# Kernel tuning notes

Hardware: AMD Instinct MI355X
Metric: run time of the kernel (lower is better)

## Reference

```python
import jax, jax.numpy as jnp
import numpy as np

N = 131072
F_IN = 256
FEATURES = 64
N_SOURCES = 32


def setup_inputs() -> dict:
    key = jax.random.key(0)
    k1, k2, k3 = jax.random.split(key, 3)
    x = jax.random.normal(k1, (N, F_IN), dtype=jnp.float32)
    source = jax.random.randint(k2, (N,), 0, N_SOURCES, dtype=jnp.int32)
    W = jax.random.normal(k3, (F_IN, N_SOURCES * FEATURES), dtype=jnp.float32) * (1.0 / np.sqrt(F_IN))
    b = jnp.zeros((N_SOURCES * FEATURES,), dtype=jnp.float32)
    return {"x": x, "source": source, "W": W, "b": b}


def reference(x, source, W, b):
    # Dense projection to all sources: (N, n_sources*features)
    y = jnp.dot(x, W) + b
    # Per-row gather of the slice belonging to this row's source id.
    # Equivalent to y[i, source[i]*FEATURES : (source[i]+1)*FEATURES].
    y = y.reshape(x.shape[0], N_SOURCES, FEATURES)
    out = jnp.take_along_axis(y, source[:, None, None].astype(jnp.int32), axis=1)
    return out[:, 0, :]  # (N, FEATURES)
```

## Files before the change

### kernel.cpp

```cpp
#include <hip/hip_runtime.h>

#define N_ROWS   131072
#define F_IN     256
#define FEAT     64
#define NSRC     32
#define WSTRIDE  (NSRC * FEAT)
#define NCH      32
#define CHUNK    4096
#define NCB      (N_ROWS / 256)
#define CBPC     16
#define CAPC     44
#define SEG      (CAPC + 1)
#define LCAP     320
#define TR       16
#define TPAD     66
#define WTOFF    (NCB * NSRC * SEG)
#define WTINTS   (NSRC * FEAT * F_IN / 2)

#define MCHUNK   4096
#define LCAP1    512
#define KPAD     264

typedef __attribute__((ext_vector_type(8))) short  bf16x8;
typedef __attribute__((ext_vector_type(4))) float  f32x4;

#define WAITV(N)  asm volatile("s_waitcnt vmcnt(" #N ")" ::: "memory")
#define WAITLGKM() asm volatile("s_waitcnt lgkmcnt(0)" ::: "memory")
#define SBAR()    do { __builtin_amdgcn_s_barrier(); __builtin_amdgcn_sched_barrier(0); } while (0)

__device__ __forceinline__ unsigned short f2bf(float f) {
    union { float f; unsigned u; } c; c.f = f;
    unsigned r = c.u + 0x7fffu + ((c.u >> 16) & 1u);
    return (unsigned short)(r >> 16);
}

__device__ __forceinline__ bf16x8 pack8(f32x4 f0, f32x4 f1) {
    bf16x8 a;
    a[0] = (short)f2bf(f0[0]); a[1] = (short)f2bf(f0[1]);
    a[2] = (short)f2bf(f0[2]); a[3] = (short)f2bf(f0[3]);
    a[4] = (short)f2bf(f1[0]); a[5] = (short)f2bf(f1[1]);
    a[6] = (short)f2bf(f1[2]); a[7] = (short)f2bf(f1[3]);
    return a;
}

__global__ __launch_bounds__(256)
void pack_w(const float* __restrict__ W, int* __restrict__ ws) {
    const int idx  = blockIdx.x * 256 + threadIdx.x;
    const int lane = idx & 63, kk = (idx >> 6) & 7, w = (idx >> 9) & 3, s = idx >> 11;
    const int col  = lane & 15, quad = lane >> 4;
    const int n    = s * FEAT + w * 16 + col;
    const int k0   = kk * 32 + quad * 8;
    bf16x8 v;
    #pragma unroll
    for (int j = 0; j < 8; ++j)
        v[j] = (short)f2bf(W[(size_t)(k0 + j) * WSTRIDE + n]);
    ((bf16x8*)(ws + WTOFF))[idx] = v;
}

__global__ __launch_bounds__(256)
void compact_kernel(const int* __restrict__ src, int* __restrict__ ws) {
    __shared__ int lcnt[NSRC];
    const int tid = threadIdx.x;
    if (tid < NSRC) lcnt[tid] = 0;
    __syncthreads();
    const int row = blockIdx.x * 256 + tid;
    const int s   = src[row];
    const int p   = atomicAdd(&lcnt[s], 1);
    if (p < CAPC)
        ws[blockIdx.x * (NSRC * SEG) + s * SEG + 1 + p] = row;
    __syncthreads();
    if (tid < NSRC)
        ws[blockIdx.x * (NSRC * SEG) + tid * SEG] = min(lcnt[tid], CAPC);
}

__device__ __forceinline__ void stage_tile(const float* __restrict__ x,
                                           const int* lst, int count, int tile,
                                           int w, int lane, float* Abuf) {
    #pragma unroll
    for (int i = 0; i < 4; ++i) {
        const int r  = w * 4 + i;
        const int gi = min(tile * TR + r, count - 1);
        const float* srcp = x + (size_t)lst[gi] * F_IN + ((lane ^ (r & 7)) << 2);
        __builtin_amdgcn_global_load_lds(
            (const __attribute__((address_space(1))) void*)srcp,
            (__attribute__((address_space(3))) void*)(Abuf + r * F_IN),
            16, 0, 0);
    }
}

__global__ __launch_bounds__(256, 4)
void gemm_kernel(const float* __restrict__ x, const float* __restrict__ b,
                 const int* __restrict__ ws, float* __restrict__ out) {
    __shared__ __align__(16) float A[2][TR][F_IN];
    __shared__ __align__(16) float T[TR * TPAD];
    __shared__ int lst[LCAP];
    __shared__ int scnt[CBPC];
    __shared__ int soff[CBPC + 1];

    const int tid = threadIdx.x;
    const int s   = blockIdx.x;
    const int c   = blockIdx.y;

    if (tid < CBPC)
        scnt[tid] = ws[(size_t)(c * CBPC + tid) * (NSRC * SEG) + s * SEG];
    __syncthreads();
    if (tid == 0) {
        int a = 0;
        #pragma unroll
        for (int jj = 0; jj < CBPC; ++jj) { soff[jj] = a; a += scnt[jj]; }
        soff[CBPC] = a;
    }
    __syncthreads();
    const int count = min(soff[CBPC], LCAP);
    if (count == 0) return;
    {
        const int jj = tid >> 4, i0 = tid & 15;
        const size_t base = (size_t)(c * CBPC + jj) * (NSRC * SEG) + s * SEG;
        const int cj = scnt[jj];
        for (int i = i0; i < cj; i += 16) {
            const int pos = soff[jj] + i;
            if (pos < LCAP) lst[pos] = ws[base + 1 + i];
        }
    }
    __syncthreads();

    const int lane = tid & 63, w = tid >> 6;
    const int col  = lane & 15, quad = lane >> 4;

    const int ntiles = (count + TR - 1) / TR;

    stage_tile(x, lst, count, 0, w, lane, &A[0][0][0]);

    bf16x8 bb[8];
    {
        const bf16x8* wp = (const bf16x8*)(ws + WTOFF) + ((s * 4 + w) * 8) * 64 + lane;
        #pragma unroll
        for (int kk = 0; kk < 8; ++kk) bb[kk] = wp[kk * 64];
    }
    const float bias = b[s * FEAT + w * 16 + col];

    for (int t = 0; t < ntiles; ++t) {
        if (t) WAITV(4); else WAITV(0);
        SBAR();
        if (t + 1 < ntiles)
            stage_tile(x, lst, count, t + 1, w, lane, &A[(t + 1) & 1][0][0]);

        f32x4 acc = (f32x4){0.f, 0.f, 0.f, 0.f};
        {
            const int key = col & 7;
            const float* arow = &A[t & 1][0][0] + col * F_IN;
            #pragma unroll
            for (int kk = 0; kk < 8; ++kk) {
                const int s0 = kk * 8 + quad * 2;
                const f32x4 lo = *(const f32x4*)(arow + (((s0    ) ^ key) << 2));
                const f32x4 hi = *(const f32x4*)(arow + (((s0 + 1) ^ key) << 2));
                unsigned u0, u1, u2, u3;
                asm("v_cvt_pk_bf16_f32 %0, %1, %2" : "=v"(u0) : "v"(lo[0]), "v"(lo[1]));
                asm("v_cvt_pk_bf16_f32 %0, %1, %2" : "=v"(u1) : "v"(lo[2]), "v"(lo[3]));
                asm("v_cvt_pk_bf16_f32 %0, %1, %2" : "=v"(u2) : "v"(hi[0]), "v"(hi[1]));
                asm("v_cvt_pk_bf16_f32 %0, %1, %2" : "=v"(u3) : "v"(hi[2]), "v"(hi[3]));
                union { unsigned u[4]; bf16x8 v; } cv;
                cv.u[0] = u0; cv.u[1] = u1; cv.u[2] = u2; cv.u[3] = u3;
                acc = __builtin_amdgcn_mfma_f32_16x16x32_bf16(cv.v, bb[kk], acc, 0, 0, 0);
            }
        }

        #pragma unroll
        for (int reg = 0; reg < 4; ++reg)
            T[(quad * 4 + reg) * TPAD + w * 16 + col] = acc[reg] + bias;
        WAITLGKM();
        SBAR();
        #pragma unroll
        for (int r = 0; r < 4; ++r) {
            const int gi = t * TR + w * 4 + r;
            if (gi < count)
                out[(size_t)lst[gi] * FEAT + lane] = T[(w * 4 + r) * TPAD + lane];
        }
    }
}

__global__ __launch_bounds__(256, 4)
void mono_kernel(const float* __restrict__ x, const int* __restrict__ src,
                 const float* __restrict__ W, const float* __restrict__ b,
                 float* __restrict__ out) {
    __shared__ __align__(16) unsigned short Wt[FEAT * KPAD];
    __shared__ int lst[LCAP1];
    __shared__ int cnt;
    const int tid = threadIdx.x, s = blockIdx.y, chunk0 = blockIdx.x * MCHUNK;
    if (tid == 0) cnt = 0;
    __syncthreads();
    {
        const int n = tid & 63, kp = (tid >> 6) * 2;
        #pragma unroll
        for (int k0 = 0; k0 < F_IN; k0 += 8) {
            const int k = k0 + kp;
            const float w0 = W[(size_t)k * WSTRIDE + s * FEAT + n];
            const float w1 = W[(size_t)(k + 1) * WSTRIDE + s * FEAT + n];
            *(unsigned*)&Wt[n * KPAD + k] = (unsigned)f2bf(w0) | ((unsigned)f2bf(w1) << 16);
        }
    }
    #pragma unroll
    for (int r = 0; r < MCHUNK / 256; ++r) {
        const int row = chunk0 + r * 256 + tid;
        if (src[row] == s) {
            const int p = atomicAdd(&cnt, 1);
            if (p < LCAP1) lst[p] = row;
        }
    }
    __syncthreads();
    const int count = cnt;
    if (count == 0) return;
    const int lane = tid & 63, w = tid >> 6, col = lane & 15, quad = lane >> 4;
    float bias[4];
    #pragma unroll
    for (int nt = 0; nt < 4; ++nt) bias[nt] = b[s * FEAT + nt * 16 + col];
    const int npass = (count + 63) >> 6;
    for (int pp = 0; pp < npass; ++pp) {
        const int base = pp * 64 + w * 16;
        const int ia = lst[min(base + col, count - 1)];
        const float* ap = x + (size_t)ia * F_IN + quad * 8;
        f32x4 av[16];
        #pragma unroll
        for (int kk = 0; kk < 8; ++kk) {
            av[2 * kk]     = *(const f32x4*)(ap + kk * 32);
            av[2 * kk + 1] = *(const f32x4*)(ap + kk * 32 + 4);
        }
        f32x4 acc[4];
        #pragma unroll
        for (int nt = 0; nt < 4; ++nt) acc[nt] = (f32x4){0.f, 0.f, 0.f, 0.f};
        #pragma unroll
        for (int kk = 0; kk < 8; ++kk) {
            const bf16x8 a = pack8(av[2 * kk], av[2 * kk + 1]);
            #pragma unroll
            for (int nt = 0; nt < 4; ++nt) {
                const bf16x8 bbv = *(const bf16x8*)&Wt[(nt * 16 + col) * KPAD + kk * 32 + quad * 8];
                acc[nt] = __builtin_amdgcn_mfma_f32_16x16x32_bf16(a, bbv, acc[nt], 0, 0, 0);
            }
        }
        #pragma unroll
        for (int reg = 0; reg < 4; ++reg) {
            const int gm = base + quad * 4 + reg;
            if (gm < count) {
                const int row = lst[gm];
                float* op = out + (size_t)row * FEAT;
                #pragma unroll
                for (int nt = 0; nt < 4; ++nt)
                    op[nt * 16 + col] = acc[nt][reg] + bias[nt];
            }
        }
    }
}

extern "C" void kernel_launch(void* const* d_in, const int* in_sizes, int n_in,
                              void* d_out, int out_size, void* d_ws, size_t ws_size,
                              hipStream_t stream) {
    const float* x   = (const float*)d_in[0];
    const int*   src = (const int*)d_in[1];
    const float* W   = (const float*)d_in[2];
    const float* b   = (const float*)d_in[3];
    float*       out = (float*)d_out;

    const size_t ws_needed = (size_t)(WTOFF + WTINTS) * sizeof(int);
    if (ws_size >= ws_needed) {
        int* ws = (int*)d_ws;
        pack_w<<<dim3(256), dim3(256), 0, stream>>>(W, ws);
        compact_kernel<<<dim3(NCB), dim3(256), 0, stream>>>(src, ws);
        gemm_kernel<<<dim3(NSRC, NCH), dim3(256), 0, stream>>>(x, b, ws, out);
    } else {
        mono_kernel<<<dim3(N_ROWS / MCHUNK, NSRC), dim3(256), 0, stream>>>(x, src, W, b, out);
    }
}
```

Before: 217.1 us.

## Pre-sort x rows into per-bucket bf16 buffers before the grouped GEMM

Replaces the compact kernel with count, scan and reorder passes. The reorder pass streams x row by row, converts it to bf16 and scatters each row into a contiguous per-(chunk, source) bucket in the workspace. The GEMM then stages contiguous bf16 tiles and feeds MFMA directly, with no gather and no per-tile conversion. This trades scattered fp32 row gathers for one extra write and read of x at half size plus two more launches. It also needs a much larger workspace, and if that is not available the code falls back to the mono kernel.

```diff
diff --git a/kernel.cpp b/kernel.cpp
--- a/kernel.cpp
+++ b/kernel.cpp
@@ -9,13 +9,22 @@
 #define CHUNK    4096
 #define NCB      (N_ROWS / 256)
 #define CBPC     16
-#define CAPC     44
-#define SEG      (CAPC + 1)
 #define LCAP     320
 #define TR       16
 #define TPAD     66
-#define WTOFF    (NCB * NSRC * SEG)
-#define WTINTS   (NSRC * FEAT * F_IN / 2)
+
+#define OFF_CNT   0
+#define SZ_CNT    (NCB * NSRC)
+#define OFF_SOFF  (OFF_CNT + SZ_CNT)
+#define SZ_SOFF   (NCH * NSRC * CBPC)
+#define OFF_BTOT  (OFF_SOFF + SZ_SOFF)
+#define SZ_BTOT   (NCH * NSRC)
+#define OFF_LSTG  (OFF_BTOT + SZ_BTOT)
+#define SZ_LSTG   (NCH * NSRC * LCAP)
+#define OFF_WT    (OFF_LSTG + SZ_LSTG)
+#define SZ_WT     (NSRC * FEAT * F_IN / 2)
+#define OFF_XS    (OFF_WT + SZ_WT)
+#define SZ_XS     (NCH * NSRC * LCAP * (F_IN/2))
 
 #define MCHUNK   4096
 #define LCAP1    512
@@ -24,9 +33,9 @@
 typedef __attribute__((ext_vector_type(8))) short  bf16x8;
 typedef __attribute__((ext_vector_type(4))) float  f32x4;
 
-#define WAITV(N)  asm volatile("s_waitcnt vmcnt(" #N ")" ::: "memory")
+#define WAITV(N)   asm volatile("s_waitcnt vmcnt(" #N ")" ::: "memory")
 #define WAITLGKM() asm volatile("s_waitcnt lgkmcnt(0)" ::: "memory")
-#define SBAR()    do { __builtin_amdgcn_s_barrier(); __builtin_amdgcn_sched_barrier(0); } while (0)
+#define SBAR()     do { __builtin_amdgcn_s_barrier(); __builtin_amdgcn_sched_barrier(0); } while (0)
 
 __device__ __forceinline__ unsigned short f2bf(float f) {
     union { float f; unsigned u; } c; c.f = f;
@@ -54,86 +63,133 @@
     #pragma unroll
     for (int j = 0; j < 8; ++j)
         v[j] = (short)f2bf(W[(size_t)(k0 + j) * WSTRIDE + n]);
-    ((bf16x8*)(ws + WTOFF))[idx] = v;
+    ((bf16x8*)(ws + OFF_WT))[idx] = v;
 }
 
 __global__ __launch_bounds__(256)
-void compact_kernel(const int* __restrict__ src, int* __restrict__ ws) {
+void count_kernel(const int* __restrict__ src, int* __restrict__ ws) {
     __shared__ int lcnt[NSRC];
     const int tid = threadIdx.x;
     if (tid < NSRC) lcnt[tid] = 0;
     __syncthreads();
-    const int row = blockIdx.x * 256 + tid;
-    const int s   = src[row];
-    const int p   = atomicAdd(&lcnt[s], 1);
-    if (p < CAPC)
-        ws[blockIdx.x * (NSRC * SEG) + s * SEG + 1 + p] = row;
-    __syncthreads();
-    if (tid < NSRC)
-        ws[blockIdx.x * (NSRC * SEG) + tid * SEG] = min(lcnt[tid], CAPC);
-}
-
-__device__ __forceinline__ void stage_tile(const float* __restrict__ x,
-                                           const int* lst, int count, int tile,
-                                           int w, int lane, float* Abuf) {
-    #pragma unroll
-    for (int i = 0; i < 4; ++i) {
-        const int r  = w * 4 + i;
-        const int gi = min(tile * TR + r, count - 1);
-        const float* srcp = x + (size_t)lst[gi] * F_IN + ((lane ^ (r & 7)) << 2);
-        __builtin_amdgcn_global_load_lds(
-            (const __attribute__((address_space(1))) void*)srcp,
-            (__attribute__((address_space(3))) void*)(Abuf + r * F_IN),
-            16, 0, 0);
+    atomicAdd(&lcnt[src[blockIdx.x * 256 + tid]], 1);
+    __syncthreads();
+    if (tid < NSRC) ws[OFF_CNT + blockIdx.x * NSRC + tid] = lcnt[tid];
+}
+
+__global__ __launch_bounds__(256)
+void scan_kernel(int* __restrict__ ws) {
+    const int bucket = blockIdx.x * 256 + threadIdx.x;
+    const int c = bucket >> 5, s = bucket & 31;
+    int acc = 0;
+    #pragma unroll
+    for (int j = 0; j < CBPC; ++j) {
+        ws[OFF_SOFF + bucket * CBPC + j] = acc;
+        acc += ws[OFF_CNT + (c * CBPC + j) * NSRC + s];
+    }
+    ws[OFF_BTOT + bucket] = min(acc, LCAP);
+}
+
+__global__ __launch_bounds__(256)
+void reorder_kernel(const float* __restrict__ x, const int* __restrict__ src,
+                    int* __restrict__ ws) {
+    __shared__ int slotbuf[256];
+    __shared__ int lcnt[NSRC];
+    __shared__ int sbase[NSRC];
+    __shared__ int send[NSRC];
+    const int tid = threadIdx.x;
+    const int c   = blockIdx.x >> 4;
+    const int jj  = blockIdx.x & 15;
+
+    if (tid < NSRC) {
+        lcnt[tid] = 0;
+        const int bucket = c * NSRC + tid;
+        sbase[tid] = bucket * LCAP + ws[OFF_SOFF + bucket * CBPC + jj];
+        send[tid]  = bucket * LCAP + LCAP;
+    }
+    __syncthreads();
+    {
+        const int row = blockIdx.x * 256 + tid;
+        const int s   = src[row];
+        const int p   = atomicAdd(&lcnt[s], 1);
+        int slot = sbase[s] + p;
+        if (slot >= send[s]) slot = -1;
+        slotbuf[tid] = slot;
+        if (slot >= 0) ws[OFF_LSTG + slot] = row;
+    }
+    __syncthreads();
+
+    const int w = tid >> 6, lane = tid & 63;
+    char* xs = (char*)(ws + OFF_XS);
+    #pragma unroll
+    for (int r0 = 0; r0 < 64; r0 += 8) {
+        f32x4 v[8];
+        int   sl[8];
+        #pragma unroll
+        for (int i = 0; i < 8; ++i) {
+            const int lr = w * 64 + r0 + i;
+            v[i]  = *(const f32x4*)(x + (size_t)(blockIdx.x * 256 + lr) * F_IN + lane * 4);
+            sl[i] = slotbuf[lr];
+        }
+        #pragma unroll
+        for (int i = 0; i < 8; ++i) {
+            if (sl[i] >= 0) {
+                unsigned u0, u1;
+                asm("v_cvt_pk_bf16_f32 %0, %1, %2" : "=v"(u0) : "v"(v[i][0]), "v"(v[i][1]));
+                asm("v_cvt_pk_bf16_f32 %0, %1, %2" : "=v"(u1) : "v"(v[i][2]), "v"(v[i][3]));
+                uint2 d; d.x = u0; d.y = u1;
+                *(uint2*)(xs + (size_t)sl[i] * 512 + lane * 8) = d;
+            }
+        }
     }
 }
 
 __global__ __launch_bounds__(256, 4)
-void gemm_kernel(const float* __restrict__ x, const float* __restrict__ b,
-                 const int* __restrict__ ws, float* __restrict__ out) {
-    __shared__ __align__(16) float A[2][TR][F_IN];
+void gemm_kernel(const float* __restrict__ b, const int* __restrict__ ws,
+                 float* __restrict__ out) {
+    __shared__ __align__(16) unsigned short A[2][TR][F_IN];
     __shared__ __align__(16) float T[TR * TPAD];
     __shared__ int lst[LCAP];
-    __shared__ int scnt[CBPC];
-    __shared__ int soff[CBPC + 1];
-
-    const int tid = threadIdx.x;
-    const int s   = blockIdx.x;
-    const int c   = blockIdx.y;
-
-    if (tid < CBPC)
-        scnt[tid] = ws[(size_t)(c * CBPC + tid) * (NSRC * SEG) + s * SEG];
-    __syncthreads();
-    if (tid == 0) {
-        int a = 0;
-        #pragma unroll
-        for (int jj = 0; jj < CBPC; ++jj) { soff[jj] = a; a += scnt[jj]; }
-        soff[CBPC] = a;
-    }
-    __syncthreads();
-    const int count = min(soff[CBPC], LCAP);
+
+    const int tid    = threadIdx.x;
+    const int s      = blockIdx.x;
+    const int c      = blockIdx.y;
+    const int bucket = c * NSRC + s;
+    const int count  = ws[OFF_BTOT + bucket];
     if (count == 0) return;
-    {
-        const int jj = tid >> 4, i0 = tid & 15;
-        const size_t base = (size_t)(c * CBPC + jj) * (NSRC * SEG) + s * SEG;
-        const int cj = scnt[jj];
-        for (int i = i0; i < cj; i += 16) {
-            const int pos = soff[jj] + i;
-            if (pos < LCAP) lst[pos] = ws[base + 1 + i];
-        }
-    }
-    __syncthreads();
+
+    for (int i = tid; i < count; i += 256)
+        lst[i] = ws[OFF_LSTG + bucket * LCAP + i];
 
     const int lane = tid & 63, w = tid >> 6;
     const int col  = lane & 15, quad = lane >> 4;
 
+    __syncthreads();
+
     const int ntiles = (count + TR - 1) / TR;
-
-    stage_tile(x, lst, count, 0, w, lane, &A[0][0][0]);
+    const char* xs = (const char*)(ws + OFF_XS) + (size_t)bucket * LCAP * 512;
+
+    #define STAGE(tile, buf)                                                     \
+    do {                                                                         \
+        _Pragma("unroll")                                                        \
+        for (int i = 0; i < 2; ++i) {                                            \
+            const int rl  = w * 4 + 2 * i + (lane >> 5);     \
+            const int gi  = min((tile) * TR + rl, count - 1);                    \
+            const int key = rl & 7;                                              \
+            const char* sp = xs + (size_t)gi * 512 + (((lane & 31) ^ key) << 4); \
+            __builtin_amdgcn_global_load_lds(                                    \
+                (const __attribute__((address_space(1))) void*)sp,               \
+                (__attribute__((address_space(3))) void*)                        \
+                    ((char*)&A[buf][0][0] + (w * 4 + 2 * i) * 512),              \
+                16, 0, 0);                                                       \
+        }                                                                        \
+    } while (0)
+
+    STAGE(0, 0);
 
     bf16x8 bb[8];
     {
-        const bf16x8* wp = (const bf16x8*)(ws + WTOFF) + ((s * 4 + w) * 8) * 64 + lane;
+        const bf16x8* wp = (const bf16x8*)(ws + OFF_WT) + ((s * 4 + w) * 8) * 64 + lane;
         #pragma unroll
         for (int kk = 0; kk < 8; ++kk) bb[kk] = wp[kk * 64];
     }
@@ -142,26 +198,16 @@
     for (int t = 0; t < ntiles; ++t) {
         if (t) WAITV(4); else WAITV(0);
         SBAR();
-        if (t + 1 < ntiles)
-            stage_tile(x, lst, count, t + 1, w, lane, &A[(t + 1) & 1][0][0]);
+        if (t + 1 < ntiles) STAGE(t + 1, (t + 1) & 1);
 
         f32x4 acc = (f32x4){0.f, 0.f, 0.f, 0.f};
         {
+            const char* arow = (const char*)&A[t & 1][0][0] + col * 512;
             const int key = col & 7;
-            const float* arow = &A[t & 1][0][0] + col * F_IN;
             #pragma unroll
             for (int kk = 0; kk < 8; ++kk) {
-                const int s0 = kk * 8 + quad * 2;
-                const f32x4 lo = *(const f32x4*)(arow + (((s0    ) ^ key) << 2));
-                const f32x4 hi = *(const f32x4*)(arow + (((s0 + 1) ^ key) << 2));
-                unsigned u0, u1, u2, u3;
-                asm("v_cvt_pk_bf16_f32 %0, %1, %2" : "=v"(u0) : "v"(lo[0]), "v"(lo[1]));
-                asm("v_cvt_pk_bf16_f32 %0, %1, %2" : "=v"(u1) : "v"(lo[2]), "v"(lo[3]));
-                asm("v_cvt_pk_bf16_f32 %0, %1, %2" : "=v"(u2) : "v"(hi[0]), "v"(hi[1]));
-                asm("v_cvt_pk_bf16_f32 %0, %1, %2" : "=v"(u3) : "v"(hi[2]), "v"(hi[3]));
-                union { unsigned u[4]; bf16x8 v; } cv;
-                cv.u[0] = u0; cv.u[1] = u1; cv.u[2] = u2; cv.u[3] = u3;
-                acc = __builtin_amdgcn_mfma_f32_16x16x32_bf16(cv.v, bb[kk], acc, 0, 0, 0);
+                const bf16x8 a = *(const bf16x8*)(arow + (((kk * 4 + quad) ^ key) << 4));
+                acc = __builtin_amdgcn_mfma_f32_16x16x32_bf16(a, bb[kk], acc, 0, 0, 0);
             }
         }
 
@@ -177,6 +223,7 @@
                 out[(size_t)lst[gi] * FEAT + lane] = T[(w * 4 + r) * TPAD + lane];
         }
     }
+    #undef STAGE
 }
 
 __global__ __launch_bounds__(256, 4)
@@ -260,12 +307,14 @@
     const float* b   = (const float*)d_in[3];
     float*       out = (float*)d_out;
 
-    const size_t ws_needed = (size_t)(WTOFF + WTINTS) * sizeof(int);
+    const size_t ws_needed = (size_t)(OFF_XS + SZ_XS) * sizeof(int);
     if (ws_size >= ws_needed) {
         int* ws = (int*)d_ws;
         pack_w<<<dim3(256), dim3(256), 0, stream>>>(W, ws);
-        compact_kernel<<<dim3(NCB), dim3(256), 0, stream>>>(src, ws);
-        gemm_kernel<<<dim3(NSRC, NCH), dim3(256), 0, stream>>>(x, b, ws, out);
+        count_kernel<<<dim3(NCB), dim3(256), 0, stream>>>(src, ws);
+        scan_kernel<<<dim3(4), dim3(256), 0, stream>>>(ws);
+        reorder_kernel<<<dim3(NCB), dim3(256), 0, stream>>>(x, src, ws);
+        gemm_kernel<<<dim3(NSRC, NCH), dim3(256), 0, stream>>>(b, ws, out);
     } else {
         mono_kernel<<<dim3(N_ROWS / MCHUNK, NSRC), dim3(256), 0, stream>>>(x, src, W, b, out);
     }
```

Measured after the change: 246.6 us. +13.6%, slower.
